# Performance work log

Measured on AMD Instinct MI355X. Metric: run time of the kernel, lower is better.

## Reference

```python
import jax, jax.numpy as jnp
import numpy as np

HIDDEN = 128
N_ING = 20000
N_CMP = 10000
N_EDGE = 1000000


def setup_inputs() -> dict:
    key = jax.random.key(0)
    k1, k2, k3, k4, k5, k6, k7 = jax.random.split(key, 7)
    x_ingredient = jax.random.normal(k1, (N_ING, HIDDEN), dtype=jnp.float32)
    x_compound = jax.random.normal(k2, (N_CMP, HIDDEN), dtype=jnp.float32)
    src_idx = jax.random.randint(k3, (N_EDGE,), 0, N_ING)
    dst_idx = jax.random.randint(k4, (N_EDGE,), 0, N_CMP)
    edge_index = jnp.stack([src_idx, dst_idx], axis=0)  # [2, E]
    # Linear(2H, H) then Linear(H, 1), PyTorch default init scale ~ 1/sqrt(fan_in)
    s1 = 1.0 / np.sqrt(2 * HIDDEN)
    s2 = 1.0 / np.sqrt(HIDDEN)
    W1 = jax.random.uniform(k5, (2 * HIDDEN, HIDDEN), dtype=jnp.float32, minval=-s1, maxval=s1)
    b1 = jax.random.uniform(k6, (HIDDEN,), dtype=jnp.float32, minval=-s1, maxval=s1)
    W2 = jax.random.uniform(k7, (HIDDEN, 1), dtype=jnp.float32, minval=-s2, maxval=s2)
    b2 = jnp.zeros((1,), dtype=jnp.float32)
    return {"x_ingredient": x_ingredient, "x_compound": x_compound,
            "edge_index": edge_index, "W1": W1, "b1": b1, "W2": W2, "b2": b2}


def reference(x_ingredient, x_compound, edge_index, W1, b1, W2, b2):
    src = x_ingredient[edge_index[0]]  # [E, H] gather
    dst = x_compound[edge_index[1]]    # [E, H] gather
    h = jnp.concatenate([src, dst], axis=-1)          # [E, 2H]
    h = jax.nn.relu(jnp.dot(h, W1) + b1)              # [E, H]
    out = jax.nn.sigmoid(jnp.dot(h, W2) + b2)         # [E, 1]
    return out
```

## Files before the change

kernel.cpp:

```cpp
#include <hip/hip_runtime.h>


#define H  128
#define NI 20000
#define NC 10000
#define NE 1000000

typedef _Float16 half8   __attribute__((ext_vector_type(8)));
typedef float    floatx2 __attribute__((ext_vector_type(2)));
typedef float    floatx4 __attribute__((ext_vector_type(4)));

#define P8_OFF    0
#define Q8_OFF    (NI * H)
#define WFRAG_B   ((NI + NC) * H)

#define PB (NI / 16)
#define QB (NC / 16)

#if __has_builtin(__builtin_amdgcn_cvt_pk_f32_fp8) && __has_builtin(__builtin_amdgcn_cvt_pk_fp8_f32)
#define HW_FP8 1
#else
#define HW_FP8 0
__device__ inline unsigned char enc_e4m3(float x) {
    unsigned s = x < 0.0f ? 0x80u : 0u;
    float a = fminf(fabsf(x), 448.0f);
    if (a < 0.0009765625f) return (unsigned char)s;
    int e; float m = frexpf(a, &e);
    int E = e + 6;
    if (E <= 0) {
        int f = (int)rintf(a * 512.0f);
        if (f > 7) return (unsigned char)(s | 0x08);
        return (unsigned char)(s | f);
    }
    int f = (int)rintf((m * 2.0f - 1.0f) * 8.0f);
    if (f == 8) { f = 0; ++E; }
    if (E > 15 || (E == 15 && f > 6)) { E = 15; f = 6; }
    return (unsigned char)(s | (E << 3) | f);
}
__device__ inline float dec_e4m3(unsigned char b) {
    int E = (b >> 3) & 15, f = b & 7;
    float v = (E == 0) ? (float)f * 0.001953125f
                       : (float)(8 + f) * exp2f((float)(E - 10));
    return (b & 0x80) ? -v : v;
}
#endif

__launch_bounds__(256)
__global__ void cvt_w(const float* __restrict__ W1,
                      unsigned char* __restrict__ wsb) {
    const int flat = blockIdx.x * 256 + threadIdx.x;
    const int j    = flat & 7;
    const int lane = (flat >> 3) & 63;
    const int ks   = (flat >> 9) & 3;
    const int ntw  = (flat >> 11) & 7;
    const int isQ  = (flat >> 14) & 1;
    const int n = (ntw >> 1) * 32 + (ntw & 1) * 16 + (lane & 15);
    const int k = isQ * 128 + ks * 32 + (lane >> 4) * 8 + j;
    ((_Float16*)(wsb + WFRAG_B))[flat] = (_Float16)W1[k * H + n];
}

__launch_bounds__(256)
__global__ void pq_gemm(const float* __restrict__ xin,
                        const float* __restrict__ xcmp,
                        const float* __restrict__ b1,
                        unsigned char* __restrict__ wsb) {
    const int b    = blockIdx.x;
    const bool isQ = (b >= PB);
    const int  rb  = (isQ ? b - PB : b) * 16;
    const float* X = isQ ? xcmp : xin;
    unsigned char* OUT8 = wsb + (isQ ? Q8_OFF : P8_OFF);
    const _Float16* wfrag = (const _Float16*)(wsb + WFRAG_B);

    const int lane = threadIdx.x & 63;
    const int w    = threadIdx.x >> 6;
    const int quad = lane >> 4;
    const int m    = lane & 15;

    half8 bf[2][4];
    float b1v[2];
#pragma unroll
    for (int nt = 0; nt < 2; ++nt) {
        const int ntw = w * 2 + nt;
#pragma unroll
        for (int ks = 0; ks < 4; ++ks)
            bf[nt][ks] = *(const half8*)(wfrag + (((isQ ? 8 : 0) + ntw) * 4 + ks) * 512 + lane * 8);
        const int n = w * 32 + nt * 16 + m;
        b1v[nt] = isQ ? b1[n] : 0.0f;
    }

    half8 af[4];
    const float* xr = X + (long)(rb + m) * H + quad * 8;
#pragma unroll
    for (int ks = 0; ks < 4; ++ks) {
        float4 a = *(const float4*)(xr + ks * 32);
        float4 c = *(const float4*)(xr + ks * 32 + 4);
        half8 v = { (_Float16)a.x, (_Float16)a.y, (_Float16)a.z, (_Float16)a.w,
                    (_Float16)c.x, (_Float16)c.y, (_Float16)c.z, (_Float16)c.w };
        af[ks] = v;
    }

    floatx4 acc[2] = { (floatx4)0.0f, (floatx4)0.0f };
#pragma unroll
    for (int ks = 0; ks < 4; ++ks)
#pragma unroll
        for (int nt = 0; nt < 2; ++nt)
            acc[nt] = __builtin_amdgcn_mfma_f32_16x16x32_f16(af[ks], bf[nt][ks], acc[nt], 0, 0, 0);

#pragma unroll
    for (int nt = 0; nt < 2; ++nt) {
        const int col = w * 32 + nt * 16 + m;
#pragma unroll
        for (int r = 0; r < 4; ++r) {
            const float v = acc[nt][r] + b1v[nt];
#if HW_FP8
            const unsigned u = (unsigned)__builtin_amdgcn_cvt_pk_fp8_f32(v, v, 0, false);
            OUT8[(rb + quad * 4 + r) * H + col] = (unsigned char)(u & 0xff);
#else
            OUT8[(rb + quad * 4 + r) * H + col] = enc_e4m3(v);
#endif
        }
    }
}

#define EGRID 2048

__launch_bounds__(256)
__global__ void edge_mlp(const unsigned char* __restrict__ wsb,
                         const int* __restrict__ src_idx,
                         const int* __restrict__ dst_idx,
                         const float* __restrict__ W2,
                         const float* __restrict__ b2p,
                         float* __restrict__ out) {
    const int tid  = threadIdx.x;
    const int c    = tid & 7;
    const int slot = tid >> 3;

    float4 w2v[4];
#pragma unroll
    for (int i = 0; i < 4; ++i) w2v[i] = *(const float4*)(W2 + c * 16 + i * 4);
    const float b2v = b2p[0];

    const unsigned char* P8 = wsb + P8_OFF;
    const unsigned char* Q8 = wsb + Q8_OFF;

    int e  = blockIdx.x * 32 + slot;
    int si = 0, di = 0;
    if (e < NE) { si = src_idx[e]; di = dst_idx[e]; }

    while (e < NE) {
        const uint4 pd = *(const uint4*)(P8 + si * H + c * 16);
        const uint4 qd = *(const uint4*)(Q8 + di * H + c * 16);

        const int e2 = e + 32 * EGRID;
        int si2 = 0, di2 = 0;
        if (e2 < NE) { si2 = src_idx[e2]; di2 = dst_idx[e2]; }

        float acc = 0.0f;
        const unsigned pw[4] = { pd.x, pd.y, pd.z, pd.w };
        const unsigned qw[4] = { qd.x, qd.y, qd.z, qd.w };
#pragma unroll
        for (int jw = 0; jw < 4; ++jw) {
#if HW_FP8
            floatx2 pl = __builtin_amdgcn_cvt_pk_f32_fp8((int)pw[jw], false);
            floatx2 ph = __builtin_amdgcn_cvt_pk_f32_fp8((int)pw[jw], true);
            floatx2 ql = __builtin_amdgcn_cvt_pk_f32_fp8((int)qw[jw], false);
            floatx2 qh = __builtin_amdgcn_cvt_pk_f32_fp8((int)qw[jw], true);
#else
            floatx2 pl = { dec_e4m3(pw[jw] & 0xff), dec_e4m3((pw[jw] >> 8) & 0xff) };
            floatx2 ph = { dec_e4m3((pw[jw] >> 16) & 0xff), dec_e4m3(pw[jw] >> 24) };
            floatx2 ql = { dec_e4m3(qw[jw] & 0xff), dec_e4m3((qw[jw] >> 8) & 0xff) };
            floatx2 qh = { dec_e4m3((qw[jw] >> 16) & 0xff), dec_e4m3(qw[jw] >> 24) };
#endif
            const float4 wv = w2v[jw];
            acc = fmaf(fmaxf(pl.x + ql.x, 0.0f), wv.x, acc);
            acc = fmaf(fmaxf(pl.y + ql.y, 0.0f), wv.y, acc);
            acc = fmaf(fmaxf(ph.x + qh.x, 0.0f), wv.z, acc);
            acc = fmaf(fmaxf(ph.y + qh.y, 0.0f), wv.w, acc);
        }

        acc += __shfl_xor(acc, 1);
        acc += __shfl_xor(acc, 2);
        acc += __shfl_xor(acc, 4);

        if (c == 0)
            out[e] = 1.0f / (1.0f + expf(-(acc + b2v)));

        e = e2; si = si2; di = di2;
    }
}

extern "C" void kernel_launch(void* const* d_in, const int* in_sizes, int n_in,
                              void* d_out, int out_size, void* d_ws, size_t ws_size,
                              hipStream_t stream) {
    const float* xin  = (const float*)d_in[0];
    const float* xcmp = (const float*)d_in[1];
    const int*   eidx = (const int*)d_in[2];
    const float* W1   = (const float*)d_in[3];
    const float* b1   = (const float*)d_in[4];
    const float* W2   = (const float*)d_in[5];
    const float* b2   = (const float*)d_in[6];
    float* out = (float*)d_out;
    unsigned char* wsb = (unsigned char*)d_ws;

    hipLaunchKernelGGL(cvt_w,   dim3(128),     dim3(256), 0, stream, W1, wsb);
    hipLaunchKernelGGL(pq_gemm, dim3(PB + QB), dim3(256), 0, stream, xin, xcmp, b1, wsb);
    hipLaunchKernelGGL(edge_mlp, dim3(EGRID),  dim3(256), 0, stream,
                       wsb, eidx, eidx + NE, W2, b2, out);
}
```

Before: 114.5 us.

## Deepen edge gather pipeline and vectorize packed relu-FMA accumulation

```diff
diff --git a/kernel.cpp b/kernel.cpp
--- a/kernel.cpp
+++ b/kernel.cpp
@@ -44,6 +44,16 @@
     return (b & 0x80) ? -v : v;
 }
 #endif
+
+__device__ inline floatx2 relu2(floatx2 v) {
+#if __has_builtin(__builtin_elementwise_max)
+    floatx2 z = {0.0f, 0.0f};
+    return __builtin_elementwise_max(v, z);
+#else
+    floatx2 r = { fmaxf(v.x, 0.0f), fmaxf(v.y, 0.0f) };
+    return r;
+#endif
+}
 
 __launch_bounds__(256)
 __global__ void cvt_w(const float* __restrict__ W1,
@@ -135,29 +145,44 @@
     const int c    = tid & 7;
     const int slot = tid >> 3;
 
-    float4 w2v[4];
-#pragma unroll
-    for (int i = 0; i < 4; ++i) w2v[i] = *(const float4*)(W2 + c * 16 + i * 4);
+    floatx2 w2v[8];
+#pragma unroll
+    for (int i = 0; i < 8; ++i) w2v[i] = *(const floatx2*)(W2 + c * 16 + i * 2);
     const float b2v = b2p[0];
 
     const unsigned char* P8 = wsb + P8_OFF;
     const unsigned char* Q8 = wsb + Q8_OFF;
-
-    int e  = blockIdx.x * 32 + slot;
-    int si = 0, di = 0;
-    if (e < NE) { si = src_idx[e]; di = dst_idx[e]; }
-
-    while (e < NE) {
-        const uint4 pd = *(const uint4*)(P8 + si * H + c * 16);
-        const uint4 qd = *(const uint4*)(Q8 + di * H + c * 16);
-
-        const int e2 = e + 32 * EGRID;
+    const int estep = 32 * EGRID;
+
+    int e0 = blockIdx.x * 32 + slot;
+    int si0 = 0, di0 = 0;
+    if (e0 < NE) {
+        si0 = __builtin_nontemporal_load(src_idx + e0);
+        di0 = __builtin_nontemporal_load(dst_idx + e0);
+    }
+    uint4 pd0 = *(const uint4*)(P8 + si0 * H + c * 16);
+    uint4 qd0 = *(const uint4*)(Q8 + di0 * H + c * 16);
+
+    int e1 = e0 + estep;
+    int si1 = 0, di1 = 0;
+    if (e1 < NE) {
+        si1 = __builtin_nontemporal_load(src_idx + e1);
+        di1 = __builtin_nontemporal_load(dst_idx + e1);
+    }
+
+    while (e0 < NE) {
+        uint4 pd1 = *(const uint4*)(P8 + si1 * H + c * 16);
+        uint4 qd1 = *(const uint4*)(Q8 + di1 * H + c * 16);
+        const int e2 = e1 + estep;
         int si2 = 0, di2 = 0;
-        if (e2 < NE) { si2 = src_idx[e2]; di2 = dst_idx[e2]; }
-
-        float acc = 0.0f;
-        const unsigned pw[4] = { pd.x, pd.y, pd.z, pd.w };
-        const unsigned qw[4] = { qd.x, qd.y, qd.z, qd.w };
+        if (e2 < NE) {
+            si2 = __builtin_nontemporal_load(src_idx + e2);
+            di2 = __builtin_nontemporal_load(dst_idx + e2);
+        }
+
+        floatx2 acc2 = {0.0f, 0.0f};
+        const unsigned pw[4] = { pd0.x, pd0.y, pd0.z, pd0.w };
+        const unsigned qw[4] = { qd0.x, qd0.y, qd0.z, qd0.w };
 #pragma unroll
         for (int jw = 0; jw < 4; ++jw) {
 #if HW_FP8
@@ -171,21 +196,22 @@
             floatx2 ql = { dec_e4m3(qw[jw] & 0xff), dec_e4m3((qw[jw] >> 8) & 0xff) };
             floatx2 qh = { dec_e4m3((qw[jw] >> 16) & 0xff), dec_e4m3(qw[jw] >> 24) };
 #endif
-            const float4 wv = w2v[jw];
-            acc = fmaf(fmaxf(pl.x + ql.x, 0.0f), wv.x, acc);
-            acc = fmaf(fmaxf(pl.y + ql.y, 0.0f), wv.y, acc);
-            acc = fmaf(fmaxf(ph.x + qh.x, 0.0f), wv.z, acc);
-            acc = fmaf(fmaxf(ph.y + qh.y, 0.0f), wv.w, acc);
-        }
+            acc2 += relu2(pl + ql) * w2v[2 * jw];
+            acc2 += relu2(ph + qh) * w2v[2 * jw + 1];
+        }
+        float acc = acc2.x + acc2.y;
 
         acc += __shfl_xor(acc, 1);
         acc += __shfl_xor(acc, 2);
         acc += __shfl_xor(acc, 4);
 
-        if (c == 0)
-            out[e] = 1.0f / (1.0f + expf(-(acc + b2v)));
-
-        e = e2; si = si2; di = di2;
+        if (c == 0) {
+            const float r = 1.0f / (1.0f + expf(-(acc + b2v)));
+            __builtin_nontemporal_store(r, out + e0);
+        }
+
+        e0 = e1; pd0 = pd1; qd0 = qd1;
+        e1 = e2; si1 = si2; di1 = di2;
     }
 }
 
```

Measured after the change: 113.9 us. No clear change (-0.5%).

## Software-pipeline edge gathers two edges deep with packed math and fast sigmoid

Applied to the files above, without the earlier changes.

```diff
diff --git a/kernel.cpp b/kernel.cpp
--- a/kernel.cpp
+++ b/kernel.cpp
@@ -44,6 +44,25 @@
     return (b & 0x80) ? -v : v;
 }
 #endif
+
+__device__ inline floatx2 relu2(floatx2 v) {
+#if __has_builtin(__builtin_elementwise_max)
+    floatx2 z = {0.0f, 0.0f};
+    return __builtin_elementwise_max(v, z);
+#else
+    floatx2 r = { fmaxf(v.x, 0.0f), fmaxf(v.y, 0.0f) };
+    return r;
+#endif
+}
+
+__device__ __forceinline__ float fast_sigmoid(float x) {
+#if __has_builtin(__builtin_amdgcn_exp2f) && __has_builtin(__builtin_amdgcn_rcpf)
+    const float t = __builtin_amdgcn_exp2f(-1.4426950408889634f * x);
+    return __builtin_amdgcn_rcpf(1.0f + t);
+#else
+    return 1.0f / (1.0f + __expf(-x));
+#endif
+}
 
 __launch_bounds__(256)
 __global__ void cvt_w(const float* __restrict__ W1,
@@ -123,6 +142,7 @@
 }
 
 #define EGRID 2048
+#define ESTEP (32 * EGRID)
 
 __launch_bounds__(256)
 __global__ void edge_mlp(const unsigned char* __restrict__ wsb,
@@ -135,58 +155,94 @@
     const int c    = tid & 7;
     const int slot = tid >> 3;
 
-    float4 w2v[4];
-#pragma unroll
-    for (int i = 0; i < 4; ++i) w2v[i] = *(const float4*)(W2 + c * 16 + i * 4);
+    floatx2 w2v[8];
+#pragma unroll
+    for (int i = 0; i < 8; ++i) w2v[i] = *(const floatx2*)(W2 + c * 16 + i * 2);
     const float b2v = b2p[0];
 
     const unsigned char* P8 = wsb + P8_OFF;
     const unsigned char* Q8 = wsb + Q8_OFF;
-
-    int e  = blockIdx.x * 32 + slot;
-    int si = 0, di = 0;
-    if (e < NE) { si = src_idx[e]; di = dst_idx[e]; }
-
-    while (e < NE) {
-        const uint4 pd = *(const uint4*)(P8 + si * H + c * 16);
-        const uint4 qd = *(const uint4*)(Q8 + di * H + c * 16);
-
-        const int e2 = e + 32 * EGRID;
-        int si2 = 0, di2 = 0;
-        if (e2 < NE) { si2 = src_idx[e2]; di2 = dst_idx[e2]; }
-
-        float acc = 0.0f;
-        const unsigned pw[4] = { pd.x, pd.y, pd.z, pd.w };
-        const unsigned qw[4] = { qd.x, qd.y, qd.z, qd.w };
-#pragma unroll
-        for (int jw = 0; jw < 4; ++jw) {
+    const int ebase = blockIdx.x * 32 + slot;
+
+#define LDIDX(K, SI, DI) do {                                        \
+        int _e = ebase + (K) * ESTEP;                                \
+        _e = _e < NE ? _e : NE - 1;                                  \
+        SI = __builtin_nontemporal_load(src_idx + _e);               \
+        DI = __builtin_nontemporal_load(dst_idx + _e);               \
+    } while (0)
+
+#define GATHER(SI, DI, PD, QD) do {                                  \
+        PD = *(const uint4*)(P8 + (SI) * H + c * 16);                \
+        QD = *(const uint4*)(Q8 + (DI) * H + c * 16);                \
+    } while (0)
+
+#define COMPUTE(K, PD, QD, MASKED) do {                              \
+        floatx2 acc2 = {0.0f, 0.0f};                                 \
+        const unsigned pw[4] = { PD.x, PD.y, PD.z, PD.w };           \
+        const unsigned qw[4] = { QD.x, QD.y, QD.z, QD.w };           \
+        _Pragma("unroll")                                            \
+        for (int jw = 0; jw < 4; ++jw) {                             \
+            floatx2 pl, ph, ql, qh;                                  \
+            DECODE(pw[jw], qw[jw], pl, ph, ql, qh);                  \
+            acc2 += relu2(pl + ql) * w2v[2 * jw];                    \
+            acc2 += relu2(ph + qh) * w2v[2 * jw + 1];                \
+        }                                                            \
+        float acc = acc2.x + acc2.y;                                 \
+        acc += __shfl_xor(acc, 1);                                   \
+        acc += __shfl_xor(acc, 2);                                   \
+        acc += __shfl_xor(acc, 4);                                   \
+        const int _e = ebase + (K) * ESTEP;                          \
+        if (c == 0 && (!(MASKED) || _e < NE)) {                      \
+            const float r = fast_sigmoid(acc + b2v);                 \
+            __builtin_nontemporal_store(r, out + _e);                \
+        }                                                            \
+    } while (0)
+
 #if HW_FP8
-            floatx2 pl = __builtin_amdgcn_cvt_pk_f32_fp8((int)pw[jw], false);
-            floatx2 ph = __builtin_amdgcn_cvt_pk_f32_fp8((int)pw[jw], true);
-            floatx2 ql = __builtin_amdgcn_cvt_pk_f32_fp8((int)qw[jw], false);
-            floatx2 qh = __builtin_amdgcn_cvt_pk_f32_fp8((int)qw[jw], true);
-#else
-            floatx2 pl = { dec_e4m3(pw[jw] & 0xff), dec_e4m3((pw[jw] >> 8) & 0xff) };
-            floatx2 ph = { dec_e4m3((pw[jw] >> 16) & 0xff), dec_e4m3(pw[jw] >> 24) };
-            floatx2 ql = { dec_e4m3(qw[jw] & 0xff), dec_e4m3((qw[jw] >> 8) & 0xff) };
-            floatx2 qh = { dec_e4m3((qw[jw] >> 16) & 0xff), dec_e4m3(qw[jw] >> 24) };
-#endif
-            const float4 wv = w2v[jw];
-            acc = fmaf(fmaxf(pl.x + ql.x, 0.0f), wv.x, acc);
-            acc = fmaf(fmaxf(pl.y + ql.y, 0.0f), wv.y, acc);
-            acc = fmaf(fmaxf(ph.x + qh.x, 0.0f), wv.z, acc);
-            acc = fmaf(fmaxf(ph.y + qh.y, 0.0f), wv.w, acc);
-        }
-
-        acc += __shfl_xor(acc, 1);
-        acc += __shfl_xor(acc, 2);
-        acc += __shfl_xor(acc, 4);
-
-        if (c == 0)
-            out[e] = 1.0f / (1.0f + expf(-(acc + b2v)));
-
-        e = e2; si = si2; di = di2;
-    }
+#define DECODE(PW, QW, PL, PH, QL, QH) do {                          \
+        PL = __builtin_amdgcn_cvt_pk_f32_fp8((int)(PW), false);      \
+        PH = __builtin_amdgcn_cvt_pk_f32_fp8((int)(PW), true);       \
+        QL = __builtin_amdgcn_cvt_pk_f32_fp8((int)(QW), false);      \
+        QH = __builtin_amdgcn_cvt_pk_f32_fp8((int)(QW), true);       \
+    } while (0)
+#else
+#define DECODE(PW, QW, PL, PH, QL, QH) do {                          \
+        PL = { dec_e4m3((PW) & 0xff), dec_e4m3(((PW) >> 8) & 0xff) };  \
+        PH = { dec_e4m3(((PW) >> 16) & 0xff), dec_e4m3((PW) >> 24) };  \
+        QL = { dec_e4m3((QW) & 0xff), dec_e4m3(((QW) >> 8) & 0xff) };  \
+        QH = { dec_e4m3(((QW) >> 16) & 0xff), dec_e4m3((QW) >> 24) };  \
+    } while (0)
+#endif
+
+    int siA, diA, siB, diB, si2, di2, si3, di3;
+    uint4 pdA, qdA, pdB, qdB;
+    LDIDX(0, siA, diA);
+    LDIDX(1, siB, diB);
+    GATHER(siA, diA, pdA, qdA);
+    GATHER(siB, diB, pdB, qdB);
+    LDIDX(2, si2, di2);
+    LDIDX(3, si3, di3);
+
+#pragma unroll 1
+    for (int i = 0; i < 7; ++i) {
+        const int k = 2 * i;
+        uint4 pdC, qdC, pdD, qdD;
+        GATHER(si2, di2, pdC, qdC);
+        GATHER(si3, di3, pdD, qdD);
+        LDIDX(k + 4, si2, di2);
+        LDIDX(k + 5, si3, di3);
+        COMPUTE(k,     pdA, qdA, false);
+        COMPUTE(k + 1, pdB, qdB, false);
+        pdA = pdC; qdA = qdC; pdB = pdD; qdB = qdD;
+    }
+
+    COMPUTE(14, pdA, qdA, false);
+    COMPUTE(15, pdB, qdB, true);
+
+#undef LDIDX
+#undef GATHER
+#undef COMPUTE
+#undef DECODE
 }
 
 extern "C" void kernel_launch(void* const* d_in, const int* in_sizes, int n_in,
```

Result: faster. 112.0 us (-2.2%).
